# Kernel optimization log

Hardware: AMD Instinct MI355X
Metric: run time of the kernel (lower is better)

## Reference

```python
import jax, jax.numpy as jnp
import numpy as np

N = 100000
E = 1600000
IN_DIM = 128
OUT_DIM = 128
H = 4
HD = OUT_DIM // H  # 32
NEG_SLOPE = 0.2
EPS_SOFTMAX = 1e-8
EPS_LN = 1e-5


def setup_inputs() -> dict:
    key = jax.random.key(0)
    ks = jax.random.split(key, 6)
    h = jax.random.normal(ks[0], (N, IN_DIM), dtype=jnp.float32)
    edge_index = jax.random.randint(ks[1], (2, E), 0, N, dtype=jnp.int32)
    W = jax.random.normal(ks[2], (IN_DIM, OUT_DIM), dtype=jnp.float32) / np.sqrt(IN_DIM)
    W_self = jax.random.normal(ks[3], (IN_DIM, OUT_DIM), dtype=jnp.float32) / np.sqrt(IN_DIM)
    a_in = jax.random.normal(ks[4], (H, 2 * HD), dtype=jnp.float32) * 0.01
    a_out = jax.random.normal(ks[5], (H, 2 * HD), dtype=jnp.float32) * 0.01
    bias = jnp.zeros((OUT_DIM,), dtype=jnp.float32)
    ln_gamma = jnp.ones((OUT_DIM,), dtype=jnp.float32)
    ln_beta = jnp.zeros((OUT_DIM,), dtype=jnp.float32)
    return {"h": h, "edge_index": edge_index, "W": W, "W_self": W_self,
            "a_in": a_in, "a_out": a_out, "bias": bias,
            "ln_gamma": ln_gamma, "ln_beta": ln_beta}


def _attention_aggregate(h_proj, sender, receiver, attn_vec, num_nodes):
    # h_proj: (N, H, HD); sender/receiver: (E,); attn_vec: (H, 2*HD)
    h_sender = h_proj[sender]      # (E, H, HD)
    h_receiver = h_proj[receiver]  # (E, H, HD)
    # e = sum over concat([h_sender, h_receiver]) * attn_vec, split halves
    e = (jnp.einsum('ehd,hd->eh', h_sender, attn_vec[:, :HD])
         + jnp.einsum('ehd,hd->eh', h_receiver, attn_vec[:, HD:]))
    e = jax.nn.leaky_relu(e, NEG_SLOPE)
    e_max = jax.ops.segment_max(e, receiver, num_segments=num_nodes)  # (N, H)
    alpha = jnp.exp(e - e_max[receiver])
    alpha_sum = jax.ops.segment_sum(alpha, receiver, num_segments=num_nodes)
    alpha = alpha / (alpha_sum[receiver] + EPS_SOFTMAX)
    msg = h_sender * alpha[..., None]  # (E, H, HD)
    return jax.ops.segment_sum(msg, receiver, num_segments=num_nodes)  # (N, H, HD)


def reference(h, edge_index, W, W_self, a_in, a_out, bias, ln_gamma, ln_beta):
    n = h.shape[0]
    h_proj = (h @ W).reshape(n, H, HD)
    h_self = h @ W_self
    src, dst = edge_index[0], edge_index[1]
    h_in = _attention_aggregate(h_proj, src, dst, a_in, n)   # 'in' direction
    h_out = _attention_aggregate(h_proj, dst, src, a_out, n)  # 'out' direction
    combined = h_self + h_in.reshape(n, -1) + h_out.reshape(n, -1) + bias
    mean = combined.mean(axis=-1, keepdims=True)
    var = combined.var(axis=-1, keepdims=True)
    normed = (combined - mean) * jax.lax.rsqrt(var + EPS_LN)
    return normed * ln_gamma + ln_beta
```

## Files before the change

### kernel.cpp

```cpp
#include <hip/hip_runtime.h>
#include <math.h>

#define HEADS 4
#define HD 32
#define DIM 128
#define NEG_SLOPE 0.2f
#define EPS_SM 1e-8f
#define EPS_LN 1e-5f
#define SH1 9
#define PB 128
#define BCOLS 272

typedef _Float16 h2_t __attribute__((ext_vector_type(2)));
typedef _Float16 f16x8 __attribute__((ext_vector_type(8)));
typedef float f32x4 __attribute__((ext_vector_type(4)));

__device__ __forceinline__ float lrelu(float x) { return x > 0.f ? x : NEG_SLOPE * x; }
__device__ __forceinline__ unsigned pkh(float a, float b) {
    return __builtin_bit_cast(unsigned, __builtin_amdgcn_cvt_pkrtz(a, b));
}
__device__ __forceinline__ float dot2(unsigned a, unsigned b, float c) {
    return __builtin_amdgcn_fdot2(__builtin_bit_cast(h2_t, a), __builtin_bit_cast(h2_t, b), c, false);
}
__device__ __forceinline__ float lo16(unsigned u) { return (float)__builtin_bit_cast(h2_t, u)[0]; }
__device__ __forceinline__ float hi16(unsigned u) { return (float)__builtin_bit_cast(h2_t, u)[1]; }

template<int LIM> __device__ __forceinline__ void rmax4(float& a, float& b, float& c, float& d) {
#pragma unroll
    for (int s = 1; s < LIM; s <<= 1) {
        a = fmaxf(a, __shfl_xor(a, s, 64));
        b = fmaxf(b, __shfl_xor(b, s, 64));
        c = fmaxf(c, __shfl_xor(c, s, 64));
        d = fmaxf(d, __shfl_xor(d, s, 64));
    }
}
template<int LIM> __device__ __forceinline__ void rsum4(float& a, float& b, float& c, float& d) {
#pragma unroll
    for (int s = 1; s < LIM; s <<= 1) {
        a += __shfl_xor(a, s, 64);
        b += __shfl_xor(b, s, 64);
        c += __shfl_xor(c, s, 64);
        d += __shfl_xor(d, s, 64);
    }
}

__device__ __forceinline__ void aggr_pairs(int cnt, const int* __restrict__ sdw,
                                           const uint2* __restrict__ wtw,
                                           const char* __restrict__ hpb,
                                           unsigned rowoff, int q, bool hlo, unsigned wsel,
                                           float (&acc)[8]) {
    const int npair = (cnt + 7) >> 3;
#pragma unroll 2
    for (int t = 0; t < npair; ++t) {
        int pi = 4 * t + q;
        uint2 sp = *(const uint2*)&sdw[2 * pi];
        uint4 wp = *(const uint4*)&wtw[2 * pi];
        uint4 u = *(const uint4*)(hpb + (((unsigned)sp.x << 8) + rowoff));
        uint4 v = *(const uint4*)(hpb + (((unsigned)sp.y << 8) + rowoff));
        unsigned wA = hlo ? wp.x : wp.y;
        unsigned wB = hlo ? wp.z : wp.w;
        unsigned wpk = __builtin_amdgcn_perm(wB, wA, wsel);
        acc[0] = dot2(__builtin_amdgcn_perm(v.x, u.x, 0x05040100u), wpk, acc[0]);
        acc[1] = dot2(__builtin_amdgcn_perm(v.x, u.x, 0x07060302u), wpk, acc[1]);
        acc[2] = dot2(__builtin_amdgcn_perm(v.y, u.y, 0x05040100u), wpk, acc[2]);
        acc[3] = dot2(__builtin_amdgcn_perm(v.y, u.y, 0x07060302u), wpk, acc[3]);
        acc[4] = dot2(__builtin_amdgcn_perm(v.z, u.z, 0x05040100u), wpk, acc[4]);
        acc[5] = dot2(__builtin_amdgcn_perm(v.z, u.z, 0x07060302u), wpk, acc[5]);
        acc[6] = dot2(__builtin_amdgcn_perm(v.w, u.w, 0x05040100u), wpk, acc[6]);
        acc[7] = dot2(__builtin_amdgcn_perm(v.w, u.w, 0x07060302u), wpk, acc[7]);
    }
}

__global__ __launch_bounds__(256) void part1a_k(const int* __restrict__ ei, int* __restrict__ cntmat,
                                                int E, int N, int NBIN,
                                                const float* __restrict__ W,
                                                const float* __restrict__ V,
                                                const float* __restrict__ a_in,
                                                const float* __restrict__ a_out,
                                                _Float16* __restrict__ Bt) {
    __shared__ int lcnt[512];
    const int t = threadIdx.x;
    if (blockIdx.x >= PB) {
        int c = (blockIdx.x - PB) * 2 + (t >> 7);
        int k = t & 127;
        float v;
        if (c < 128) {
            v = W[k * 128 + c];
        } else if (c < 256) {
            v = V[k * 128 + (c - 128)];
        } else {
            int d = (c - 256) >> 2, hh = (c - 256) & 3;
            const float* a = (d < 2) ? a_in : a_out;
            int base = hh * 64 + (d & 1) * 32;
            float s = 0.f;
#pragma unroll
            for (int tt = 0; tt < 32; ++tt) s += W[k * 128 + 32 * hh + tt] * a[base + tt];
            v = s;
        }
        Bt[c * 128 + k] = (_Float16)v;
        return;
    }
    const int CH = (E + PB - 1) / PB;
    const int e0 = blockIdx.x * CH;
    const int e1 = min(e0 + CH, E);
    for (int i = t; i < 512; i += 256) lcnt[i] = 0;
    __syncthreads();
    for (int e = e0 + t; e < e1; e += 256) {
        int s = ei[e], d = ei[E + e];
        atomicAdd(&lcnt[d >> SH1], 1);
        atomicAdd(&lcnt[(N + s) >> SH1], 1);
    }
    __syncthreads();
    for (int i = t; i < NBIN; i += 256) cntmat[i * PB + blockIdx.x] = lcnt[i];
}

__global__ __launch_bounds__(256) void mfma_gemm_k(const float* __restrict__ h,
                                                   const _Float16* __restrict__ Bt,
                                                   unsigned* __restrict__ hs_pk,
                                                   unsigned* __restrict__ hp_pk,
                                                   float* __restrict__ pA0, float* __restrict__ pA1,
                                                   float* __restrict__ pB0, float* __restrict__ pB1,
                                                   int N) {
    __shared__ _Float16 hs[64][128];
    __shared__ _Float16 hss[64][128];
    const int tid = threadIdx.x;
    const int w = tid >> 6, l = tid & 63;
    const int l15 = l & 15;
    const int kg = l >> 4;
    const int row0 = blockIdx.x * 64;
    const int arow = row0 + 16 * w + l15;

    f32x4 acc[17];
#pragma unroll
    for (int j = 0; j < 17; ++j) {
        acc[j][0] = 0.f; acc[j][1] = 0.f; acc[j][2] = 0.f; acc[j][3] = 0.f;
    }

    const uint4* __restrict__ bt4 = (const uint4*)Bt;

#pragma unroll
    for (int kc = 0; kc < 4; ++kc) {
        union { unsigned u[4]; f16x8 v; } cv;
        if (arow < N) {
            float4 x0 = ((const float4*)h)[(size_t)arow * 32 + kc * 8 + kg * 2];
            float4 x1 = ((const float4*)h)[(size_t)arow * 32 + kc * 8 + kg * 2 + 1];
            cv.u[0] = pkh(x0.x, x0.y); cv.u[1] = pkh(x0.z, x0.w);
            cv.u[2] = pkh(x1.x, x1.y); cv.u[3] = pkh(x1.z, x1.w);
        } else {
            cv.u[0] = 0u; cv.u[1] = 0u; cv.u[2] = 0u; cv.u[3] = 0u;
        }
        f16x8 af = cv.v;
#pragma unroll
        for (int j = 0; j < 17; ++j) {
            int col = 16 * j + l15;
            union { uint4 q; f16x8 v; } bc;
            bc.q = bt4[col * 16 + kc * 4 + kg];
            acc[j] = __builtin_amdgcn_mfma_f32_16x16x32_f16(af, bc.v, acc[j], 0, 0, 0);
        }
    }

    const int r4 = kg * 4;
    const int dsel = l15 >> 2, hh = l15 & 3;
    float* __restrict__ pd = (dsel == 0) ? pA0 : (dsel == 1) ? pA1 : (dsel == 2) ? pB0 : pB1;
#pragma unroll
    for (int r = 0; r < 4; ++r) {
        int lr = 16 * w + r4 + r;
        int grow = row0 + lr;
#pragma unroll
        for (int j = 0; j < 8; ++j)
            hs[lr][16 * j + l15] = (_Float16)acc[j][r];
#pragma unroll
        for (int j = 8; j < 16; ++j)
            hss[lr][16 * (j - 8) + l15] = (_Float16)acc[j][r];
        if (grow < N) pd[grow * 4 + hh] = acc[16][r];
    }
    __syncthreads();
    const uint4* hsv = (const uint4*)&hs[0][0];
    const uint4* hssv = (const uint4*)&hss[0][0];
#pragma unroll
    for (int p = 0; p < 4; ++p) {
        int chunk = tid + p * 256;
        int rrow = chunk >> 4, cg = chunk & 15;
        int grow = row0 + rrow;
        if (grow < N) {
            ((uint4*)hp_pk)[(size_t)grow * 16 + cg] = hsv[rrow * 16 + cg];
            ((uint4*)hs_pk)[(size_t)grow * 16 + cg] = hssv[rrow * 16 + cg];
        }
    }
}

__global__ __launch_bounds__(128) void scanB_k(const int* __restrict__ cntmat,
                                               int* __restrict__ blkoff, int* __restrict__ btot) {
    __shared__ int ls[PB];
    const int bin = blockIdx.x;
    const int t = threadIdx.x;
    int v = cntmat[bin * PB + t];
    ls[t] = v;
    __syncthreads();
#pragma unroll
    for (int d = 1; d < PB; d <<= 1) {
        int u = (t >= d) ? ls[t - d] : 0;
        __syncthreads();
        ls[t] += u;
        __syncthreads();
    }
    blkoff[bin * PB + t] = ls[t] - v;
    if (t == PB - 1) btot[bin] = ls[t];
}

__global__ __launch_bounds__(256) void scanC_k(const int* __restrict__ btot,
                                               int* __restrict__ bbase, int NBIN, int twoE) {
    __shared__ int ls[256];
    int t = threadIdx.x;
    int i0 = 2 * t, i1 = 2 * t + 1;
    int v0 = (i0 < NBIN) ? btot[i0] : 0;
    int v1 = (i1 < NBIN) ? btot[i1] : 0;
    int pair = v0 + v1;
    ls[t] = pair;
    __syncthreads();
#pragma unroll
    for (int d = 1; d < 256; d <<= 1) {
        int u = (t >= d) ? ls[t - d] : 0;
        __syncthreads();
        ls[t] += u;
        __syncthreads();
    }
    int excl = ls[t] - pair;
    if (i0 < NBIN) bbase[i0] = excl;
    if (i1 < NBIN) bbase[i1] = excl + v0;
    if (t == 0) bbase[NBIN] = twoE;
}

__global__ __launch_bounds__(256) void part1b_k(const int* __restrict__ ei,
                                                const int* __restrict__ bbase,
                                                const int* __restrict__ blkoff,
                                                unsigned* __restrict__ rec, int E, int N, int NBIN) {
    __shared__ int gb[512];
    __shared__ int lcur[512];
    const int t = threadIdx.x;
    const int CH = (E + gridDim.x - 1) / gridDim.x;
    const int e0 = blockIdx.x * CH;
    const int e1 = min(e0 + CH, E);
    for (int i = t; i < 512; i += 256) lcur[i] = 0;
    for (int i = t; i < NBIN; i += 256) gb[i] = bbase[i] + blkoff[i * PB + blockIdx.x];
    __syncthreads();
    for (int e = e0 + t; e < e1; e += 256) {
        int s = ei[e], d = ei[E + e];
        int b1 = d >> SH1;
        int r1 = atomicAdd(&lcur[b1], 1);
        rec[gb[b1] + r1] = (unsigned)s | ((unsigned)(d & 511) << 20);
        int so = N + s;
        int b2 = so >> SH1;
        int r2 = atomicAdd(&lcur[b2], 1);
        rec[gb[b2] + r2] = (unsigned)d | ((unsigned)(so & 511) << 20);
    }
}

__global__ __launch_bounds__(256) void build2_k(const unsigned* __restrict__ rec,
                                                const int* __restrict__ bbase,
                                                int* __restrict__ off, int* __restrict__ csr,
                                                int M, int twoE, int NBIN) {
    __shared__ int lcnt[512];
    __shared__ int lcur[512];
    __shared__ int ls[256];
    const int b = blockIdx.x;
    const int t = threadIdx.x;
    const int base = bbase[b];
    const int cnt = bbase[b + 1] - base;
    const int seg0 = b << SH1;
    for (int i = t; i < 512; i += 256) lcnt[i] = 0;
    __syncthreads();
    for (int k = t; k < cnt; k += 256) atomicAdd(&lcnt[rec[base + k] >> 20], 1);
    __syncthreads();
    int v0 = lcnt[2 * t], v1 = lcnt[2 * t + 1];
    int pair = v0 + v1;
    ls[t] = pair;
    __syncthreads();
#pragma unroll
    for (int d = 1; d < 256; d <<= 1) {
        int u = (t >= d) ? ls[t - d] : 0;
        __syncthreads();
        ls[t] += u;
        __syncthreads();
    }
    int excl = ls[t] - pair;
    lcur[2 * t] = excl;
    lcur[2 * t + 1] = excl + v0;
    int sg = seg0 + 2 * t;
    if (sg < M) off[sg] = base + excl;
    if (sg + 1 < M) off[sg + 1] = base + excl + v0;
    if (b == NBIN - 1 && t == 0) off[M] = twoE;
    __syncthreads();
    for (int k = t; k < cnt; k += 256) {
        unsigned r = rec[base + k];
        int pos = atomicAdd(&lcur[r >> 20], 1);
        csr[base + pos] = (int)(r & 0xFFFFFu);
    }
}

__global__ __launch_bounds__(256) void node_aggr_ln_k(const unsigned* __restrict__ hp_pk,
                                                      const unsigned* __restrict__ hs_pk,
                                                      const float* __restrict__ pA0, const float* __restrict__ pA1,
                                                      const float* __restrict__ pB0, const float* __restrict__ pB1,
                                                      const int* __restrict__ off, const int* __restrict__ csr,
                                                      const float* __restrict__ bias,
                                                      const float* __restrict__ gamma,
                                                      const float* __restrict__ beta,
                                                      float* __restrict__ out, int N) {
    __shared__ int sds[4][64];
    __shared__ uint2 wts[4][64];
    const int wave = threadIdx.x >> 6;
    const int lane = threadIdx.x & 63;
    const int n = blockIdx.x * 4 + wave;
    if (n >= N) return;
    const int l15 = lane & 15;
    const int q = lane >> 4;
    const unsigned wsel = (l15 & 4) ? 0x07060302u : 0x05040100u;
    const bool hlo = (l15 < 8);
    int* sdw = sds[wave];
    uint2* wtw = wts[wave];
    const char* hpb = (const char*)hp_pk;
    const unsigned rowoff = (unsigned)l15 << 4;

    float acc[8];
#pragma unroll
    for (int k = 0; k < 8; ++k) acc[k] = 0.f;

    const int beg0 = off[n], end0 = off[n + 1];
    const int beg1 = off[N + n], end1 = off[N + n + 1];
    const int len0 = end0 - beg0, len1 = end1 - beg1;

    if (len0 <= 32 && len1 <= 32) {
        const int half = lane >> 5;
        const int hl = lane & 31;
        const int beg = half ? beg1 : beg0;
        const int len = half ? len1 : len0;
        const float* __restrict__ pp0 = half ? pB0 : pA0;
        const float* __restrict__ pp1 = half ? pB1 : pA1;
        float4 r1 = ((const float4*)pp1)[n];
        int sid = 0;
        float e0 = -INFINITY, e1 = -INFINITY, e2 = -INFINITY, e3 = -INFINITY;
        if (hl < len) {
            sid = csr[beg + hl];
            float4 r0 = ((const float4*)pp0)[sid];
            e0 = lrelu(r0.x + r1.x);
            e1 = lrelu(r0.y + r1.y);
            e2 = lrelu(r0.z + r1.z);
            e3 = lrelu(r0.w + r1.w);
        }
        float m0 = e0, m1 = e1, m2 = e2, m3 = e3;
        const bool small16 = (len0 <= 16 && len1 <= 16);
        if (small16) rmax4<16>(m0, m1, m2, m3);
        else         rmax4<32>(m0, m1, m2, m3);
        float w0 = 0.f, w1 = 0.f, w2 = 0.f, w3 = 0.f;
        if (hl < len) {
            w0 = __expf(e0 - m0); w1 = __expf(e1 - m1);
            w2 = __expf(e2 - m2); w3 = __expf(e3 - m3);
        }
        float s0 = w0, s1 = w1, s2 = w2, s3 = w3;
        if (small16) rsum4<16>(s0, s1, s2, s3);
        else         rsum4<32>(s0, s1, s2, s3);
        w0 *= 1.f / (s0 + EPS_SM);
        w1 *= 1.f / (s1 + EPS_SM);
        w2 *= 1.f / (s2 + EPS_SM);
        w3 *= 1.f / (s3 + EPS_SM);
        sdw[lane] = 0;
        wtw[lane] = make_uint2(0u, 0u);
        if (hl < len) {
            int pos = half ? len0 + hl : hl;
            sdw[pos] = sid;
            wtw[pos] = make_uint2(pkh(w0, w1), pkh(w2, w3));
        }
        aggr_pairs(len0 + len1, sdw, wtw, hpb, rowoff, q, hlo, wsel, acc);
    } else {
#pragma unroll
        for (int dir = 0; dir < 2; ++dir) {
            const int beg = (dir == 0) ? beg0 : beg1;
            const int end = (dir == 0) ? end0 : end1;
            const int len = end - beg;
            if (len == 0) continue;
            const float* __restrict__ p0 = (dir == 0) ? pA0 : pB0;
            const float* __restrict__ p1 = (dir == 0) ? pA1 : pB1;
            float4 r1 = ((const float4*)p1)[n];

            if (len <= 64) {
                int sid = 0;
                float e0 = -INFINITY, e1 = -INFINITY, e2 = -INFINITY, e3 = -INFINITY;
                if (lane < len) {
                    sid = csr[beg + lane];
                    float4 r0 = ((const float4*)p0)[sid];
                    e0 = lrelu(r0.x + r1.x);
                    e1 = lrelu(r0.y + r1.y);
                    e2 = lrelu(r0.z + r1.z);
                    e3 = lrelu(r0.w + r1.w);
                }
                float m0 = e0, m1 = e1, m2 = e2, m3 = e3;
                rmax4<64>(m0, m1, m2, m3);
                float w0 = 0.f, w1 = 0.f, w2 = 0.f, w3 = 0.f;
                if (lane < len) {
                    w0 = __expf(e0 - m0); w1 = __expf(e1 - m1);
                    w2 = __expf(e2 - m2); w3 = __expf(e3 - m3);
                }
                float s0 = w0, s1 = w1, s2 = w2, s3 = w3;
                rsum4<64>(s0, s1, s2, s3);
                w0 *= 1.f / (s0 + EPS_SM);
                w1 *= 1.f / (s1 + EPS_SM);
                w2 *= 1.f / (s2 + EPS_SM);
                w3 *= 1.f / (s3 + EPS_SM);
                sdw[lane] = sid;
                wtw[lane] = make_uint2(pkh(w0, w1), pkh(w2, w3));
                aggr_pairs(len, sdw, wtw, hpb, rowoff, q, hlo, wsel, acc);
            } else {
                float m0 = -INFINITY, m1 = -INFINITY, m2 = -INFINITY, m3 = -INFINITY;
                for (int base = beg; base < end; base += 64) {
                    int j = base + lane;
                    if (j < end) {
                        int sid = csr[j];
                        float4 r0 = ((const float4*)p0)[sid];
                        m0 = fmaxf(m0, lrelu(r0.x + r1.x));
                        m1 = fmaxf(m1, lrelu(r0.y + r1.y));
                        m2 = fmaxf(m2, lrelu(r0.z + r1.z));
                        m3 = fmaxf(m3, lrelu(r0.w + r1.w));
                    }
                }
                rmax4<64>(m0, m1, m2, m3);
                float s0 = 0.f, s1 = 0.f, s2 = 0.f, s3 = 0.f;
                for (int base = beg; base < end; base += 64) {
                    int j = base + lane;
                    if (j < end) {
                        int sid = csr[j];
                        float4 r0 = ((const float4*)p0)[sid];
                        s0 += __expf(lrelu(r0.x + r1.x) - m0);
                        s1 += __expf(lrelu(r0.y + r1.y) - m1);
                        s2 += __expf(lrelu(r0.z + r1.z) - m2);
                        s3 += __expf(lrelu(r0.w + r1.w) - m3);
                    }
                }
                rsum4<64>(s0, s1, s2, s3);
                const float is0 = 1.f / (s0 + EPS_SM);
                const float is1 = 1.f / (s1 + EPS_SM);
                const float is2 = 1.f / (s2 + EPS_SM);
                const float is3 = 1.f / (s3 + EPS_SM);
                for (int base = beg; base < end; base += 64) {
                    int cnt = min(64, end - base);
                    int sid = 0;
                    float w0 = 0.f, w1 = 0.f, w2 = 0.f, w3 = 0.f;
                    if (lane < cnt) {
                        sid = csr[base + lane];
                        float4 r0 = ((const float4*)p0)[sid];
                        w0 = __expf(lrelu(r0.x + r1.x) - m0) * is0;
                        w1 = __expf(lrelu(r0.y + r1.y) - m1) * is1;
                        w2 = __expf(lrelu(r0.z + r1.z) - m2) * is2;
                        w3 = __expf(lrelu(r0.w + r1.w) - m3) * is3;
                    }
                    sdw[lane] = sid;
                    wtw[lane] = make_uint2(pkh(w0, w1), pkh(w2, w3));
                    aggr_pairs(cnt, sdw, wtw, hpb, rowoff, q, hlo, wsel, acc);
                }
            }
        }
    }

#pragma unroll
    for (int s = 16; s < 64; s <<= 1) {
#pragma unroll
        for (int k = 0; k < 8; ++k) acc[k] += __shfl_xor(acc[k], s, 64);
    }

    size_t bb = (size_t)n * DIM;
    uint4 hv = ((const uint4*)hs_pk)[(size_t)n * 16 + l15];
    float4 b0 = ((const float4*)bias)[2 * l15];
    float4 b1 = ((const float4*)bias)[2 * l15 + 1];
    float x0 = lo16(hv.x) + acc[0] + b0.x;
    float x1 = hi16(hv.x) + acc[1] + b0.y;
    float x2 = lo16(hv.y) + acc[2] + b0.z;
    float x3 = hi16(hv.y) + acc[3] + b0.w;
    float y0 = lo16(hv.z) + acc[4] + b1.x;
    float y1 = hi16(hv.z) + acc[5] + b1.y;
    float y2 = lo16(hv.w) + acc[6] + b1.z;
    float y3 = hi16(hv.w) + acc[7] + b1.w;
    float sum = x0 + x1 + x2 + x3 + y0 + y1 + y2 + y3;
    float sq = x0 * x0 + x1 * x1 + x2 * x2 + x3 * x3
             + y0 * y0 + y1 * y1 + y2 * y2 + y3 * y3;
#pragma unroll
    for (int m = 1; m < 64; m <<= 1) {
        sum += __shfl_xor(sum, m, 64);
        sq += __shfl_xor(sq, m, 64);
    }
    float mean = sum * (1.f / 512.f);
    float var = sq * (1.f / 512.f) - mean * mean;
    float inv = rsqrtf(var + EPS_LN);
    if (lane < 16) {
        float4 g0 = ((const float4*)gamma)[2 * l15];
        float4 g1 = ((const float4*)gamma)[2 * l15 + 1];
        float4 be0 = ((const float4*)beta)[2 * l15];
        float4 be1 = ((const float4*)beta)[2 * l15 + 1];
        float4 o0 = make_float4((x0 - mean) * inv * g0.x + be0.x,
                                (x1 - mean) * inv * g0.y + be0.y,
                                (x2 - mean) * inv * g0.z + be0.z,
                                (x3 - mean) * inv * g0.w + be0.w);
        float4 o1 = make_float4((y0 - mean) * inv * g1.x + be1.x,
                                (y1 - mean) * inv * g1.y + be1.y,
                                (y2 - mean) * inv * g1.z + be1.z,
                                (y3 - mean) * inv * g1.w + be1.w);
        ((float4*)(out + bb))[2 * l15] = o0;
        ((float4*)(out + bb))[2 * l15 + 1] = o1;
    }
}

extern "C" void kernel_launch(void* const* d_in, const int* in_sizes, int n_in,
                              void* d_out, int out_size, void* d_ws, size_t ws_size,
                              hipStream_t stream) {
    const float* h      = (const float*)d_in[0];
    const int*   ei     = (const int*)d_in[1];
    const float* W      = (const float*)d_in[2];
    const float* W_self = (const float*)d_in[3];
    const float* a_in   = (const float*)d_in[4];
    const float* a_out  = (const float*)d_in[5];
    const float* bias   = (const float*)d_in[6];
    const float* gamma  = (const float*)d_in[7];
    const float* beta   = (const float*)d_in[8];
    float* out = (float*)d_out;

    const int N = in_sizes[0] / DIM;
    const int E = in_sizes[1] / 2;
    const int M = 2 * N;
    const int NBIN = (M + (1 << SH1) - 1) >> SH1;
    const int twoE = 2 * E;

    float* ws = (float*)d_ws;
    size_t off_f = 0;
    unsigned* hs_pk = (unsigned*)(ws + off_f); off_f += (size_t)N * 64;
    unsigned* hp_pk = (unsigned*)(ws + off_f); off_f += (size_t)N * 64;
    float* pA0 = ws + off_f; off_f += (size_t)N * 4;
    float* pA1 = ws + off_f; off_f += (size_t)N * 4;
    float* pB0 = ws + off_f; off_f += (size_t)N * 4;
    float* pB1 = ws + off_f; off_f += (size_t)N * 4;
    int* ip = (int*)(ws + off_f);
    size_t off_i = 0;
    int* cntmat = ip + off_i; off_i += (size_t)NBIN * PB;
    int* blkoff = ip + off_i; off_i += (size_t)NBIN * PB;
    int* btot   = ip + off_i; off_i += NBIN;
    int* bbase  = ip + off_i; off_i += (size_t)NBIN + 1;
    int* off    = ip + off_i; off_i += (size_t)M + 1;
    unsigned* rec = (unsigned*)(ip + off_i); off_i += (size_t)twoE;
    int* csr    = ip + off_i; off_i += (size_t)twoE;
    _Float16* Bt = (_Float16*)(ip + off_i); off_i += (size_t)(BCOLS * 128) / 2;

    part1a_k<<<PB + BCOLS / 2, 256, 0, stream>>>(ei, cntmat, E, N, NBIN,
                                                 W, W_self, a_in, a_out, Bt);
    scanB_k<<<NBIN, PB, 0, stream>>>(cntmat, blkoff, btot);
    scanC_k<<<1, 256, 0, stream>>>(btot, bbase, NBIN, twoE);
    part1b_k<<<PB, 256, 0, stream>>>(ei, bbase, blkoff, rec, E, N, NBIN);
    build2_k<<<NBIN, 256, 0, stream>>>(rec, bbase, off, csr, M, twoE, NBIN);

    mfma_gemm_k<<<(N + 63) / 64, 256, 0, stream>>>(h, Bt, hs_pk, hp_pk,
                                                   pA0, pA1, pB0, pB1, N);

    node_aggr_ln_k<<<(N + 3) / 4, 256, 0, stream>>>(hp_pk, hs_pk, pA0, pA1, pB0, pB1,
                                                    off, csr, bias, gamma, beta, out, N);
}
```

Baseline: 398.1 us.

## Fuse edge scatter with GEMM, double PB, prefetch neighbor rows early

```diff
diff --git a/kernel.cpp b/kernel.cpp
--- a/kernel.cpp
+++ b/kernel.cpp
@@ -8,7 +8,7 @@
 #define EPS_SM 1e-8f
 #define EPS_LN 1e-5f
 #define SH1 9
-#define PB 128
+#define PB 256
 #define BCOLS 272
 
 typedef _Float16 h2_t __attribute__((ext_vector_type(2)));
@@ -42,6 +42,17 @@
         c += __shfl_xor(c, s, 64);
         d += __shfl_xor(d, s, 64);
     }
+}
+
+__device__ __forceinline__ void dot8(uint4 u, uint4 v, unsigned wpk, float (&acc)[8]) {
+    acc[0] = dot2(__builtin_amdgcn_perm(v.x, u.x, 0x05040100u), wpk, acc[0]);
+    acc[1] = dot2(__builtin_amdgcn_perm(v.x, u.x, 0x07060302u), wpk, acc[1]);
+    acc[2] = dot2(__builtin_amdgcn_perm(v.y, u.y, 0x05040100u), wpk, acc[2]);
+    acc[3] = dot2(__builtin_amdgcn_perm(v.y, u.y, 0x07060302u), wpk, acc[3]);
+    acc[4] = dot2(__builtin_amdgcn_perm(v.z, u.z, 0x05040100u), wpk, acc[4]);
+    acc[5] = dot2(__builtin_amdgcn_perm(v.z, u.z, 0x07060302u), wpk, acc[5]);
+    acc[6] = dot2(__builtin_amdgcn_perm(v.w, u.w, 0x05040100u), wpk, acc[6]);
+    acc[7] = dot2(__builtin_amdgcn_perm(v.w, u.w, 0x07060302u), wpk, acc[7]);
 }
 
 __device__ __forceinline__ void aggr_pairs(int cnt, const int* __restrict__ sdw,
@@ -60,14 +71,7 @@
         unsigned wA = hlo ? wp.x : wp.y;
         unsigned wB = hlo ? wp.z : wp.w;
         unsigned wpk = __builtin_amdgcn_perm(wB, wA, wsel);
-        acc[0] = dot2(__builtin_amdgcn_perm(v.x, u.x, 0x05040100u), wpk, acc[0]);
-        acc[1] = dot2(__builtin_amdgcn_perm(v.x, u.x, 0x07060302u), wpk, acc[1]);
-        acc[2] = dot2(__builtin_amdgcn_perm(v.y, u.y, 0x05040100u), wpk, acc[2]);
-        acc[3] = dot2(__builtin_amdgcn_perm(v.y, u.y, 0x07060302u), wpk, acc[3]);
-        acc[4] = dot2(__builtin_amdgcn_perm(v.z, u.z, 0x05040100u), wpk, acc[4]);
-        acc[5] = dot2(__builtin_amdgcn_perm(v.z, u.z, 0x07060302u), wpk, acc[5]);
-        acc[6] = dot2(__builtin_amdgcn_perm(v.w, u.w, 0x05040100u), wpk, acc[6]);
-        acc[7] = dot2(__builtin_amdgcn_perm(v.w, u.w, 0x07060302u), wpk, acc[7]);
+        dot8(u, v, wpk, acc);
     }
 }
 
@@ -114,20 +118,89 @@
     for (int i = t; i < NBIN; i += 256) cntmat[i * PB + blockIdx.x] = lcnt[i];
 }
 
-__global__ __launch_bounds__(256) void mfma_gemm_k(const float* __restrict__ h,
-                                                   const _Float16* __restrict__ Bt,
-                                                   unsigned* __restrict__ hs_pk,
-                                                   unsigned* __restrict__ hp_pk,
-                                                   float* __restrict__ pA0, float* __restrict__ pA1,
-                                                   float* __restrict__ pB0, float* __restrict__ pB1,
-                                                   int N) {
+__global__ __launch_bounds__(256) void scanB_k(const int* __restrict__ cntmat,
+                                               int* __restrict__ blkoff, int* __restrict__ btot) {
+    __shared__ int ls[PB];
+    const int bin = blockIdx.x;
+    const int t = threadIdx.x;
+    int v = cntmat[bin * PB + t];
+    ls[t] = v;
+    __syncthreads();
+#pragma unroll
+    for (int d = 1; d < PB; d <<= 1) {
+        int u = (t >= d) ? ls[t - d] : 0;
+        __syncthreads();
+        ls[t] += u;
+        __syncthreads();
+    }
+    blkoff[bin * PB + t] = ls[t] - v;
+    if (t == PB - 1) btot[bin] = ls[t];
+}
+
+__global__ __launch_bounds__(256) void scanC_k(const int* __restrict__ btot,
+                                               int* __restrict__ bbase, int NBIN, int twoE) {
+    __shared__ int ls[256];
+    int t = threadIdx.x;
+    int i0 = 2 * t, i1 = 2 * t + 1;
+    int v0 = (i0 < NBIN) ? btot[i0] : 0;
+    int v1 = (i1 < NBIN) ? btot[i1] : 0;
+    int pair = v0 + v1;
+    ls[t] = pair;
+    __syncthreads();
+#pragma unroll
+    for (int d = 1; d < 256; d <<= 1) {
+        int u = (t >= d) ? ls[t - d] : 0;
+        __syncthreads();
+        ls[t] += u;
+        __syncthreads();
+    }
+    int excl = ls[t] - pair;
+    if (i0 < NBIN) bbase[i0] = excl;
+    if (i1 < NBIN) bbase[i1] = excl + v0;
+    if (t == 0) bbase[NBIN] = twoE;
+}
+
+__global__ __launch_bounds__(256) void p1b_gemm_k(const int* __restrict__ ei,
+                                                  const int* __restrict__ bbase,
+                                                  const int* __restrict__ blkoff,
+                                                  unsigned* __restrict__ rec, int E, int N, int NBIN,
+                                                  const float* __restrict__ h,
+                                                  const _Float16* __restrict__ Bt,
+                                                  unsigned* __restrict__ hs_pk,
+                                                  unsigned* __restrict__ hp_pk,
+                                                  float* __restrict__ pA0, float* __restrict__ pA1,
+                                                  float* __restrict__ pB0, float* __restrict__ pB1) {
+    __shared__ int gb[512];
+    __shared__ int lcur[512];
     __shared__ _Float16 hs[64][128];
     __shared__ _Float16 hss[64][128];
+
+    if (blockIdx.x < PB) {
+        const int t = threadIdx.x;
+        const int CH = (E + PB - 1) / PB;
+        const int e0 = blockIdx.x * CH;
+        const int e1 = min(e0 + CH, E);
+        for (int i = t; i < 512; i += 256) lcur[i] = 0;
+        for (int i = t; i < NBIN; i += 256) gb[i] = bbase[i] + blkoff[i * PB + blockIdx.x];
+        __syncthreads();
+        for (int e = e0 + t; e < e1; e += 256) {
+            int s = ei[e], d = ei[E + e];
+            int b1 = d >> SH1;
+            int r1 = atomicAdd(&lcur[b1], 1);
+            rec[gb[b1] + r1] = (unsigned)s | ((unsigned)(d & 511) << 20);
+            int so = N + s;
+            int b2 = so >> SH1;
+            int r2 = atomicAdd(&lcur[b2], 1);
+            rec[gb[b2] + r2] = (unsigned)d | ((unsigned)(so & 511) << 20);
+        }
+        return;
+    }
+
     const int tid = threadIdx.x;
     const int w = tid >> 6, l = tid & 63;
     const int l15 = l & 15;
     const int kg = l >> 4;
-    const int row0 = blockIdx.x * 64;
+    const int row0 = (blockIdx.x - PB) * 64;
     const int arow = row0 + 16 * w + l15;
 
     f32x4 acc[17];
@@ -186,73 +259,6 @@
             ((uint4*)hp_pk)[(size_t)grow * 16 + cg] = hsv[rrow * 16 + cg];
             ((uint4*)hs_pk)[(size_t)grow * 16 + cg] = hssv[rrow * 16 + cg];
         }
-    }
-}
-
-__global__ __launch_bounds__(128) void scanB_k(const int* __restrict__ cntmat,
-                                               int* __restrict__ blkoff, int* __restrict__ btot) {
-    __shared__ int ls[PB];
-    const int bin = blockIdx.x;
-    const int t = threadIdx.x;
-    int v = cntmat[bin * PB + t];
-    ls[t] = v;
-    __syncthreads();
-#pragma unroll
-    for (int d = 1; d < PB; d <<= 1) {
-        int u = (t >= d) ? ls[t - d] : 0;
-        __syncthreads();
-        ls[t] += u;
-        __syncthreads();
-    }
-    blkoff[bin * PB + t] = ls[t] - v;
-    if (t == PB - 1) btot[bin] = ls[t];
-}
-
-__global__ __launch_bounds__(256) void scanC_k(const int* __restrict__ btot,
-                                               int* __restrict__ bbase, int NBIN, int twoE) {
-    __shared__ int ls[256];
-    int t = threadIdx.x;
-    int i0 = 2 * t, i1 = 2 * t + 1;
-    int v0 = (i0 < NBIN) ? btot[i0] : 0;
-    int v1 = (i1 < NBIN) ? btot[i1] : 0;
-    int pair = v0 + v1;
-    ls[t] = pair;
-    __syncthreads();
-#pragma unroll
-    for (int d = 1; d < 256; d <<= 1) {
-        int u = (t >= d) ? ls[t - d] : 0;
-        __syncthreads();
-        ls[t] += u;
-        __syncthreads();
-    }
-    int excl = ls[t] - pair;
-    if (i0 < NBIN) bbase[i0] = excl;
-    if (i1 < NBIN) bbase[i1] = excl + v0;
-    if (t == 0) bbase[NBIN] = twoE;
-}
-
-__global__ __launch_bounds__(256) void part1b_k(const int* __restrict__ ei,
-                                                const int* __restrict__ bbase,
-                                                const int* __restrict__ blkoff,
-                                                unsigned* __restrict__ rec, int E, int N, int NBIN) {
-    __shared__ int gb[512];
-    __shared__ int lcur[512];
-    const int t = threadIdx.x;
-    const int CH = (E + gridDim.x - 1) / gridDim.x;
-    const int e0 = blockIdx.x * CH;
-    const int e1 = min(e0 + CH, E);
-    for (int i = t; i < 512; i += 256) lcur[i] = 0;
-    for (int i = t; i < NBIN; i += 256) gb[i] = bbase[i] + blkoff[i * PB + blockIdx.x];
-    __syncthreads();
-    for (int e = e0 + t; e < e1; e += 256) {
-        int s = ei[e], d = ei[E + e];
-        int b1 = d >> SH1;
-        int r1 = atomicAdd(&lcur[b1], 1);
-        rec[gb[b1] + r1] = (unsigned)s | ((unsigned)(d & 511) << 20);
-        int so = N + s;
-        int b2 = so >> SH1;
-        int r2 = atomicAdd(&lcur[b2], 1);
-        rec[gb[b2] + r2] = (unsigned)d | ((unsigned)(so & 511) << 20);
     }
 }
 
@@ -298,6 +304,7 @@
     }
 }
 
+#define ROWLD(x) (*(const uint4*)(hpb + (((unsigned)(x) << 8) + rowoff)))
 __global__ __launch_bounds__(256) void node_aggr_ln_k(const unsigned* __restrict__ hp_pk,
                                                       const unsigned* __restrict__ hs_pk,
                                                       const float* __restrict__ pA0, const float* __restrict__ pA1,
@@ -340,9 +347,28 @@
         float4 r1 = ((const float4*)pp1)[n];
         int sid = 0;
         float e0 = -INFINITY, e1 = -INFINITY, e2 = -INFINITY, e3 = -INFINITY;
+        float4 r0 = make_float4(0.f, 0.f, 0.f, 0.f);
         if (hl < len) {
             sid = csr[beg + hl];
-            float4 r0 = ((const float4*)pp0)[sid];
+            r0 = ((const float4*)pp0)[sid];
+        }
+        sdw[lane] = 0;
+        wtw[lane] = make_uint2(0u, 0u);
+        if (hl < len) sdw[half ? len0 + hl : hl] = sid;
+
+        const int cnt = len0 + len1;
+        const int npair = (cnt + 7) >> 3;
+        uint4 u0 = make_uint4(0u, 0u, 0u, 0u), v0 = u0, u1 = u0, v1 = u0;
+        if (npair > 0) {
+            uint2 s = *(const uint2*)&sdw[2 * q];
+            u0 = ROWLD(s.x); v0 = ROWLD(s.y);
+        }
+        if (npair > 1) {
+            uint2 s = *(const uint2*)&sdw[2 * (4 + q)];
+            u1 = ROWLD(s.x); v1 = ROWLD(s.y);
+        }
+
+        if (hl < len) {
             e0 = lrelu(r0.x + r1.x);
             e1 = lrelu(r0.y + r1.y);
             e2 = lrelu(r0.z + r1.z);
@@ -364,14 +390,33 @@
         w1 *= 1.f / (s1 + EPS_SM);
         w2 *= 1.f / (s2 + EPS_SM);
         w3 *= 1.f / (s3 + EPS_SM);
-        sdw[lane] = 0;
-        wtw[lane] = make_uint2(0u, 0u);
-        if (hl < len) {
-            int pos = half ? len0 + hl : hl;
-            sdw[pos] = sid;
-            wtw[pos] = make_uint2(pkh(w0, w1), pkh(w2, w3));
-        }
-        aggr_pairs(len0 + len1, sdw, wtw, hpb, rowoff, q, hlo, wsel, acc);
+        if (hl < len)
+            wtw[half ? len0 + hl : hl] = make_uint2(pkh(w0, w1), pkh(w2, w3));
+
+        for (int t = 0; t < npair; t += 2) {
+            {
+                uint4 wp = *(const uint4*)&wtw[2 * (4 * t + q)];
+                unsigned wA = hlo ? wp.x : wp.y;
+                unsigned wB = hlo ? wp.z : wp.w;
+                unsigned wpk = __builtin_amdgcn_perm(wB, wA, wsel);
+                dot8(u0, v0, wpk, acc);
+            }
+            if (t + 2 < npair) {
+                uint2 s = *(const uint2*)&sdw[2 * (4 * (t + 2) + q)];
+                u0 = ROWLD(s.x); v0 = ROWLD(s.y);
+            }
+            if (t + 1 < npair) {
+                uint4 wp = *(const uint4*)&wtw[2 * (4 * (t + 1) + q)];
+                unsigned wA = hlo ? wp.x : wp.y;
+                unsigned wB = hlo ? wp.z : wp.w;
+                unsigned wpk = __builtin_amdgcn_perm(wB, wA, wsel);
+                dot8(u1, v1, wpk, acc);
+                if (t + 3 < npair) {
+                    uint2 s = *(const uint2*)&sdw[2 * (4 * (t + 3) + q)];
+                    u1 = ROWLD(s.x); v1 = ROWLD(s.y);
+                }
+            }
+        }
     } else {
 #pragma unroll
         for (int dir = 0; dir < 2; ++dir) {
@@ -547,15 +592,17 @@
     int* csr    = ip + off_i; off_i += (size_t)twoE;
     _Float16* Bt = (_Float16*)(ip + off_i); off_i += (size_t)(BCOLS * 128) / 2;
 
+    const int GB = (N + 63) / 64;
+
     part1a_k<<<PB + BCOLS / 2, 256, 0, stream>>>(ei, cntmat, E, N, NBIN,
                                                  W, W_self, a_in, a_out, Bt);
     scanB_k<<<NBIN, PB, 0, stream>>>(cntmat, blkoff, btot);
     scanC_k<<<1, 256, 0, stream>>>(btot, bbase, NBIN, twoE);
-    part1b_k<<<PB, 256, 0, stream>>>(ei, bbase, blkoff, rec, E, N, NBIN);
+
+    p1b_gemm_k<<<PB + GB, 256, 0, stream>>>(ei, bbase, blkoff, rec, E, N, NBIN,
+                                            h, Bt, hs_pk, hp_pk, pA0, pA1, pB0, pB1);
+
     build2_k<<<NBIN, 256, 0, stream>>>(rec, bbase, off, csr, M, twoE, NBIN);
-
-    mfma_gemm_k<<<(N + 63) / 64, 256, 0, stream>>>(h, Bt, hs_pk, hp_pk,
-                                                   pA0, pA1, pB0, pB1, N);
 
     node_aggr_ln_k<<<(N + 3) / 4, 256, 0, stream>>>(hp_pk, hs_pk, pA0, pA1, pB0, pB1,
                                                     off, csr, bias, gamma, beta, out, N);
```

New measurement: 372.2 us. 6.5% less time.
